# Optimization experiments

Measured on AMD Instinct MI355X. Metric: run time of the kernel, lower is better.

The kernel has to match this reference:

```python
import jax, jax.numpy as jnp
import numpy as np

B, T, C, H = 64, 256, 384, 6
HS = C // H  # 64
EPS = 1e-3  # keras LayerNormalization default epsilon


def layernorm(x, gamma, beta):
    mu = jnp.mean(x, axis=-1, keepdims=True)
    var = jnp.var(x, axis=-1, keepdims=True)
    return (x - mu) * jax.lax.rsqrt(var + EPS) * gamma + beta


def setup_inputs() -> dict:
    key = jax.random.key(0)
    ks = jax.random.split(key, 12)
    s = lambda fan_in: 1.0 / np.sqrt(fan_in)
    return {
        "x": jax.random.normal(ks[0], (B, T, C), dtype=jnp.float32),
        "Wq": jax.random.normal(ks[1], (H, C, HS), dtype=jnp.float32) * s(C),
        "Wk": jax.random.normal(ks[2], (H, C, HS), dtype=jnp.float32) * s(C),
        "Wv": jax.random.normal(ks[3], (H, C, HS), dtype=jnp.float32) * s(C),
        "Wp": jax.random.normal(ks[4], (C, C), dtype=jnp.float32) * s(C),
        "bp": jnp.zeros((C,), dtype=jnp.float32),
        "W1": jax.random.normal(ks[5], (C, 4 * C), dtype=jnp.float32) * s(C),
        "b1": jnp.zeros((4 * C,), dtype=jnp.float32),
        "W2": jax.random.normal(ks[6], (4 * C, C), dtype=jnp.float32) * s(4 * C),
        "b2": jnp.zeros((C,), dtype=jnp.float32),
        "g1": jnp.ones((C,), dtype=jnp.float32),
        "be1": jnp.zeros((C,), dtype=jnp.float32),
        "g2": jnp.ones((C,), dtype=jnp.float32),
        "be2": jnp.zeros((C,), dtype=jnp.float32),
    }


def reference(x, Wq, Wk, Wv, Wp, bp, W1, b1, W2, b2, g1, be1, g2, be2):
    # --- self-attention sub-block (dropout is identity at inference) ---
    h = layernorm(x, g1, be1)                              # [B,T,C]
    q = jnp.einsum('btc,hcd->bhtd', h, Wq)                 # [B,H,T,HS]
    k = jnp.einsum('btc,hcd->bhtd', h, Wk)
    v = jnp.einsum('btc,hcd->bhtd', h, Wv)
    scale = HS ** -0.5
    wei = jnp.einsum('bhtd,bhsd->bhts', q, k) * scale      # [B,H,T,T]
    causal = jnp.tril(jnp.ones((T, T), dtype=bool))
    wei = jnp.where(causal[None, None], wei, -jnp.inf)
    att = jax.nn.softmax(wei, axis=-1)
    o = jnp.einsum('bhts,bhsd->bthd', att, v).reshape(B, T, C)  # concat heads
    sa = o @ Wp + bp
    x = x + sa
    # --- feed-forward sub-block ---
    h2 = layernorm(x, g2, be2)
    ff = jax.nn.relu(h2 @ W1 + b1) @ W2 + b2
    return x + ff
```

## Files before the change

kernel.cpp:

```cpp
#include <hip/hip_runtime.h>
#include <hip/hip_bf16.h>
#include <math.h>

#define Bn 64
#define Tn 256
#define Cn 384
#define Hn 6
#define HSn 64
#define FFn 1536
#define EPSn 1e-3f
#define SECn 6291456

typedef __attribute__((ext_vector_type(4))) float f32x4;
typedef __attribute__((ext_vector_type(2))) float f32x2;
typedef __attribute__((ext_vector_type(8))) short short8;
typedef __attribute__((ext_vector_type(4))) short short4v;
typedef __attribute__((ext_vector_type(2))) short short2v;

__device__ __forceinline__ void async_copy16(void* lds, const void* g) {
    __builtin_amdgcn_global_load_lds(
        (const __attribute__((address_space(1))) void*)g,
        (__attribute__((address_space(3))) void*)lds, 16, 0, 0);
}

__device__ __forceinline__ short f2bf(float v) {
    __hip_bfloat16 h = __float2bfloat16(v);
    return *(short*)&h;
}


__global__ __launch_bounds__(256) void ln_pack_kernel(const float* __restrict__ x,
                                                      const float* __restrict__ g,
                                                      const float* __restrict__ be,
                                                      __hip_bfloat16* __restrict__ outPk) {
    int mt = blockIdx.x;
    int tid = threadIdx.x;
    int lane = tid & 63, wave = tid >> 6;
    __shared__ short rows[16 * 392];
#pragma unroll
    for (int i = 0; i < 4; i++) {
        int r = wave * 4 + i;
        const float* xr = x + ((size_t)mt * 16 + r) * Cn;
        f32x4 a = *(const f32x4*)(xr + lane * 4);
        f32x2 b = *(const f32x2*)(xr + 256 + lane * 2);
        float s = a.x + a.y + a.z + a.w + b.x + b.y;
#pragma unroll
        for (int off = 32; off; off >>= 1) s += __shfl_xor(s, off);
        float mu = s * (1.0f / Cn);
        f32x4 da = a - mu;
        f32x2 db = b - mu;
        float sq = da.x * da.x + da.y * da.y + da.z * da.z + da.w * da.w + db.x * db.x + db.y * db.y;
#pragma unroll
        for (int off = 32; off; off >>= 1) sq += __shfl_xor(sq, off);
        float rs = rsqrtf(sq * (1.0f / Cn) + EPSn);
        f32x4 g4 = *(const f32x4*)(g + lane * 4);
        f32x2 g2 = *(const f32x2*)(g + 256 + lane * 2);
        f32x4 e4 = *(const f32x4*)(be + lane * 4);
        f32x2 e2 = *(const f32x2*)(be + 256 + lane * 2);
        f32x4 y4 = da * rs * g4 + e4;
        f32x2 y2 = db * rs * g2 + e2;
        short4v o4 = {f2bf(y4.x), f2bf(y4.y), f2bf(y4.z), f2bf(y4.w)};
        *(short4v*)(&rows[r * 392 + lane * 4]) = o4;
        short2v o2 = {f2bf(y2.x), f2bf(y2.y)};
        *(short2v*)(&rows[r * 392 + 256 + lane * 2]) = o2;
    }
    __syncthreads();
    int r = lane & 15, q = lane >> 4;
#pragma unroll
    for (int p = 0; p < 3; p++) {
        int f = p * 4 + (tid >> 6);
        short8 v = *(const short8*)(&rows[r * 392 + f * 32 + q * 8]);
        *(short8*)((short*)outPk + ((size_t)mt * 12 + f) * 512 + lane * 8) = v;
    }
}

__global__ __launch_bounds__(256) void pack_b_kernel(const float* __restrict__ W,
                                                     __hip_bfloat16* __restrict__ out,
                                                     int K, int N) {
    int id = blockIdx.x * 256 + threadIdx.x;
    if (id >= K * N) return;
    int tile = id >> 9, lane = (id >> 3) & 63, j = id & 7;
    int ntiles = N >> 4;
    int k = (tile / ntiles) * 32 + ((lane >> 4) << 3) + j;
    int n = (tile % ntiles) * 16 + (lane & 15);
    out[id] = __float2bfloat16(W[(size_t)k * N + n]);
}

__global__ __launch_bounds__(256) void pack_qkv_kernel(const float* __restrict__ Wq,
                                                       const float* __restrict__ Wk,
                                                       const float* __restrict__ Wv,
                                                       __hip_bfloat16* __restrict__ out) {
    int id = blockIdx.x * 256 + threadIdx.x;
    if (id >= Cn * 1152) return;
    int tile = id >> 9, lane = (id >> 3) & 63, j = id & 7;
    int k = (tile / 72) * 32 + ((lane >> 4) << 3) + j;
    int n = (tile % 72) * 16 + (lane & 15);
    int sec = n / Cn, rem = n % Cn;
    int hh = rem >> 6, d = rem & 63;
    const float* W = (sec == 0) ? Wq : ((sec == 1) ? Wk : Wv);
    out[id] = __float2bfloat16(W[((size_t)hh * Cn + k) * HSn + d]);
}

template <int NN, int EPI>
__global__ __launch_bounds__(256, 3) void gemm_persist(const __hip_bfloat16* __restrict__ Apk,
                                                       const __hip_bfloat16* __restrict__ Bp,
                                                       const float* __restrict__ bias,
                                                       const float* __restrict__ resid,
                                                       float* __restrict__ outF,
                                                       __hip_bfloat16* __restrict__ outB) {
    constexpr int GX = NN / 64;
    constexpr int K32 = 12;
    constexpr int NT16 = NN / 16;
    __shared__ __align__(16) short ldsB[48 * 512];

    int l = blockIdx.x;
    int xcd = l & 7, i = l >> 3;
    int rowblk = xcd * 16 + i / GX;
    int colblk = i - (i / GX) * GX;

    int lane = threadIdx.x & 63, wave = threadIdx.x >> 6;
    int lrow = lane & 15, lquad = lane >> 4;
    int m0 = rowblk * 128;
    int n0 = colblk * 64;
    int mt0 = (m0 >> 4) + wave * 2;

    {
        const short* bbase = (const short*)Bp + (size_t)(n0 >> 4) * 512 + lane * 8;
#pragma unroll
        for (int t = 0; t < 12; t++) {
            int idx = wave * 12 + t;
            int kf = idx >> 2, ntl = idx & 3;
            async_copy16(&ldsB[idx * 512], bbase + ((size_t)kf * NT16 + ntl) * 512);
        }
    }

    f32x4 acc[2][4];
#pragma unroll
    for (int st = 0; st < 2; st++)
#pragma unroll
        for (int nt = 0; nt < 4; nt++) acc[st][nt] = (f32x4){0.f, 0.f, 0.f, 0.f};

    const short* a0p = (const short*)Apk + ((size_t)mt0 * K32) * 512 + lane * 8;
    const short* a1p = a0p + (size_t)K32 * 512;

    short8 af[2][2][3];
#pragma unroll
    for (int kf = 0; kf < 3; kf++) {
        af[0][0][kf] = *(const short8*)(a0p + kf * 512);
        af[0][1][kf] = *(const short8*)(a1p + kf * 512);
    }
    __syncthreads();

#pragma unroll
    for (int q = 0; q < 4; q++) {
        if (q < 3) {
#pragma unroll
            for (int kf = 0; kf < 3; kf++) {
                af[(q + 1) & 1][0][kf] = *(const short8*)(a0p + ((q + 1) * 3 + kf) * 512);
                af[(q + 1) & 1][1][kf] = *(const short8*)(a1p + ((q + 1) * 3 + kf) * 512);
            }
        }
#pragma unroll
        for (int kf = 0; kf < 3; kf++) {
            int kfa = q * 3 + kf;
#pragma unroll
            for (int nt = 0; nt < 4; nt++) {
                short8 bf = *(const short8*)(&ldsB[(kfa * 4 + nt) * 512 + lane * 8]);
                acc[0][nt] = __builtin_amdgcn_mfma_f32_16x16x32_bf16(af[q & 1][0][kf], bf,
                                                                     acc[0][nt], 0, 0, 0);
                acc[1][nt] = __builtin_amdgcn_mfma_f32_16x16x32_bf16(af[q & 1][1][kf], bf,
                                                                     acc[1][nt], 0, 0, 0);
            }
        }
    }
    __syncthreads();

    if (EPI == 1) {
        float* twf = (float*)((char*)ldsB + wave * 4864);
        float bnv[4];
#pragma unroll
        for (int nt = 0; nt < 4; nt++) bnv[nt] = bias[n0 + nt * 16 + lrow];
#pragma unroll
        for (int st = 0; st < 2; st++) {
            int mbase = m0 + (2 * wave + st) * 16;
#pragma unroll
            for (int nt = 0; nt < 4; nt++)
#pragma unroll
                for (int r = 0; r < 4; r++)
                    twf[(lquad * 4 + r) * 76 + nt * 16 + lrow] = acc[st][nt][r] + bnv[nt];
            int row = lane >> 2, seg = lane & 3;
            int m = mbase + row;
            const float* rrow = resid + (size_t)m * NN + n0 + seg * 16;
            float* orow = outF + (size_t)m * NN + n0 + seg * 16;
#pragma unroll
            for (int c = 0; c < 4; c++) {
                f32x4 vv = *(const f32x4*)(&twf[row * 76 + seg * 16 + c * 4]);
                f32x4 rv = *(const f32x4*)(rrow + c * 4);
                *(f32x4*)(orow + c * 4) = vv + rv;
            }
            __builtin_amdgcn_s_waitcnt(0);
        }
    } else {
        short* tws = (short*)((char*)ldsB + wave * 4864);
        float bnv[4];
        if (EPI == 2) {
#pragma unroll
            for (int nt = 0; nt < 4; nt++) bnv[nt] = bias[n0 + nt * 16 + lrow];
        }
#pragma unroll
        for (int st = 0; st < 2; st++)
#pragma unroll
            for (int nt = 0; nt < 4; nt++)
#pragma unroll
                for (int r = 0; r < 4; r++) {
                    float v = acc[st][nt][r];
                    if (EPI == 2) v = fmaxf(v + bnv[nt], 0.0f);
                    tws[(st * 16 + lquad * 4 + r) * 72 + nt * 16 + lrow] = f2bf(v);
                }
        if (EPI == 2) {
#pragma unroll
            for (int st2 = 0; st2 < 2; st2++) {
                int mt = (m0 >> 4) + wave * 2 + st2;
#pragma unroll
                for (int kcl = 0; kcl < 2; kcl++) {
                    int kc = (n0 >> 5) + kcl;
                    short8 v = *(const short8*)(
                        &tws[(st2 * 16 + (lane & 15)) * 72 + kcl * 32 + (lane >> 4) * 8]);
                    *(short8*)((short*)outB + ((size_t)mt * (NN / 32) + kc) * 512 + lane * 8) = v;
                }
            }
        } else {
            int sec = n0 / 384;
            int rem0 = n0 - sec * 384;
            int hh = rem0 >> 6;
            int b = m0 >> 8;
            int t_base = (m0 & 255) + wave * 32;
            int bh2 = b * Hn + hh;
            if (sec < 2) {
                short* outp = (short*)outB + (size_t)sec * SECn + (size_t)bh2 * 16384 +
                              (size_t)(t_base >> 4) * 1024 + lane * 8;
#pragma unroll
                for (int st2 = 0; st2 < 2; st2++)
#pragma unroll
                    for (int kc = 0; kc < 2; kc++) {
                        short8 v8 = *(const short8*)(
                            &tws[(st2 * 16 + (lane & 15)) * 72 + kc * 32 + (lane >> 4) * 8]);
                        *(short8*)(outp + (st2 * 2 + kc) * 512) = v8;
                    }
            } else {
                short* vout = (short*)outB + (size_t)2 * SECn + (size_t)bh2 * 16384 +
                              (size_t)((t_base >> 5) * 4) * 512;
#pragma unroll
                for (int dt = 0; dt < 4; dt++) {
                    short8 v8;
#pragma unroll
                    for (int j = 0; j < 8; j++) {
                        int t_loc = ((lane >> 4) << 3) + j;
                        v8[j] = tws[t_loc * 72 + dt * 16 + (lane & 15)];
                    }
                    *(short8*)(vout + dt * 512 + lane * 8) = v8;
                }
            }
        }
    }
}

template <int KK, int NN, int EPI>
__global__ __launch_bounds__(256) void gemm_mfma(const __hip_bfloat16* __restrict__ Apk,
                                                 const __hip_bfloat16* __restrict__ Bp,
                                                 const float* __restrict__ bias,
                                                 const float* __restrict__ resid,
                                                 float* __restrict__ outF,
                                                 __hip_bfloat16* __restrict__ outB) {
    constexpr int GX = NN / 64;
    constexpr int K32 = KK / 32;
    constexpr int NC = K32 / 4;
    constexpr int NT16 = NN / 16;
    __shared__ __align__(16) short ldsB[2 * 8192];

    int l = blockIdx.x;
    int xcd = l & 7, i = l >> 3;
    int rowblk = xcd * 16 + i / GX;
    int colblk = i - (i / GX) * GX;

    int lane = threadIdx.x & 63, wave = threadIdx.x >> 6;
    int lrow = lane & 15, lquad = lane >> 4;
    int m0 = rowblk * 128;
    int n0 = colblk * 64;
    int mt0 = (m0 >> 4) + wave * 2;

    f32x4 acc[2][4];
#pragma unroll
    for (int st = 0; st < 2; st++)
#pragma unroll
        for (int nt = 0; nt < 4; nt++) acc[st][nt] = (f32x4){0.f, 0.f, 0.f, 0.f};

    const short* a0p = (const short*)Apk + ((size_t)mt0 * K32) * 512 + lane * 8;
    const short* a1p = a0p + (size_t)K32 * 512;
    const short* bsrc = (const short*)Bp + ((size_t)wave * NT16 + (n0 >> 4)) * 512 + lane * 8;
    short* bdst0 = ldsB + wave * 2048;

#pragma unroll
    for (int nt = 0; nt < 4; nt++) async_copy16(bdst0 + nt * 512, bsrc + nt * 512);
    short8 aR[2][2][4];
#pragma unroll
    for (int kf = 0; kf < 4; kf++) {
        aR[0][0][kf] = *(const short8*)(a0p + kf * 512);
        aR[0][1][kf] = *(const short8*)(a1p + kf * 512);
    }

#pragma unroll
    for (int c = 0; c < NC; c++) {
        __syncthreads();
        if (c + 1 < NC) {
            const short* bs = bsrc + (size_t)(c + 1) * 4 * NT16 * 512;
            short* bd = ldsB + ((c + 1) & 1) * 8192 + wave * 2048;
#pragma unroll
            for (int nt = 0; nt < 4; nt++) async_copy16(bd + nt * 512, bs + nt * 512);
#pragma unroll
            for (int kf = 0; kf < 4; kf++) {
                aR[(c + 1) & 1][0][kf] = *(const short8*)(a0p + ((c + 1) * 4 + kf) * 512);
                aR[(c + 1) & 1][1][kf] = *(const short8*)(a1p + ((c + 1) * 4 + kf) * 512);
            }
        }
        const short* bl = ldsB + (c & 1) * 8192 + lane * 8;
#pragma unroll
        for (int kf = 0; kf < 4; kf++) {
#pragma unroll
            for (int nt = 0; nt < 4; nt++) {
                short8 bf = *(const short8*)(bl + (kf * 4 + nt) * 512);
                acc[0][nt] = __builtin_amdgcn_mfma_f32_16x16x32_bf16(aR[c & 1][0][kf], bf,
                                                                     acc[0][nt], 0, 0, 0);
                acc[1][nt] = __builtin_amdgcn_mfma_f32_16x16x32_bf16(aR[c & 1][1][kf], bf,
                                                                     acc[1][nt], 0, 0, 0);
            }
        }
    }
    __syncthreads();

    if (EPI == 1) {
        float* twf = (float*)((char*)ldsB + wave * 4864);
        float bnv[4];
#pragma unroll
        for (int nt = 0; nt < 4; nt++) bnv[nt] = bias[n0 + nt * 16 + lrow];
#pragma unroll
        for (int st = 0; st < 2; st++) {
            int mbase = m0 + (2 * wave + st) * 16;
#pragma unroll
            for (int nt = 0; nt < 4; nt++)
#pragma unroll
                for (int r = 0; r < 4; r++)
                    twf[(lquad * 4 + r) * 76 + nt * 16 + lrow] = acc[st][nt][r] + bnv[nt];
            int row = lane >> 2, seg = lane & 3;
            int m = mbase + row;
            const float* rrow = resid + (size_t)m * NN + n0 + seg * 16;
            float* orow = outF + (size_t)m * NN + n0 + seg * 16;
#pragma unroll
            for (int c = 0; c < 4; c++) {
                f32x4 vv = *(const f32x4*)(&twf[row * 76 + seg * 16 + c * 4]);
                f32x4 rv = *(const f32x4*)(rrow + c * 4);
                *(f32x4*)(orow + c * 4) = vv + rv;
            }
            __builtin_amdgcn_s_waitcnt(0);
        }
    } else {
        short* tws = (short*)((char*)ldsB + wave * 4864);
        float bnv[4];
        if (EPI == 2) {
#pragma unroll
            for (int nt = 0; nt < 4; nt++) bnv[nt] = bias[n0 + nt * 16 + lrow];
        }
#pragma unroll
        for (int st = 0; st < 2; st++)
#pragma unroll
            for (int nt = 0; nt < 4; nt++)
#pragma unroll
                for (int r = 0; r < 4; r++) {
                    float v = acc[st][nt][r];
                    if (EPI == 2) v = fmaxf(v + bnv[nt], 0.0f);
                    tws[(st * 16 + lquad * 4 + r) * 72 + nt * 16 + lrow] = f2bf(v);
                }
        if (EPI == 2) {
#pragma unroll
            for (int st2 = 0; st2 < 2; st2++) {
                int mt = (m0 >> 4) + wave * 2 + st2;
#pragma unroll
                for (int kcl = 0; kcl < 2; kcl++) {
                    int kc = (n0 >> 5) + kcl;
                    short8 v = *(const short8*)(
                        &tws[(st2 * 16 + (lane & 15)) * 72 + kcl * 32 + (lane >> 4) * 8]);
                    *(short8*)((short*)outB + ((size_t)mt * (NN / 32) + kc) * 512 + lane * 8) = v;
                }
            }
        }
    }
}

__global__ __launch_bounds__(256) void attn_mfma_kernel(const __hip_bfloat16* __restrict__ qp,
                                                        const __hip_bfloat16* __restrict__ kp,
                                                        const __hip_bfloat16* __restrict__ vp,
                                                        __hip_bfloat16* __restrict__ o) {
    __shared__ short Kl[16 * 1024];
    __shared__ short Pl[4 * 2048];
    int blk = blockIdx.x;
    int bh = blk % (Bn * Hn);
    int jg = blk / (Bn * Hn);
    int b = bh / Hn, hh = bh - b * Hn;
    int tid = threadIdx.x;
    int lane = tid & 63, wave = tid >> 6;
    int c16 = lane & 15, quad = lane >> 4;
    int qt = (wave << 2) + ((wave & 1) ? (3 - jg) : jg);

    const short* ks = (const short*)kp + (size_t)bh * 16384;
#pragma unroll
    for (int i = 0; i < 8; i++) {
        int tile = wave * 8 + i;
        async_copy16(&Kl[tile * 512], ks + tile * 512 + lane * 8);
    }

    const short* qs = (const short*)qp + (size_t)bh * 16384 + (size_t)qt * 1024 + lane * 8;
    const short* vs = (const short*)vp + (size_t)bh * 16384 + lane * 8;
    short* Pw = Pl + wave * 2048;

    short8 aq0 = *(const short8*)(qs);
    short8 aq1 = *(const short8*)(qs + 512);

    int st_max = qt;
    int kb_count = (qt + 2) >> 1;
    int covered = kb_count * 2;
    int qrow0 = qt * 16;

    __syncthreads();

    f32x4 accS[16];
#pragma unroll
    for (int st = 0; st < 16; st++) accS[st] = (f32x4){0.f, 0.f, 0.f, 0.f};
#pragma unroll
    for (int st = 0; st < 16; st++) {
        if (st <= st_max) {
            short8 bk0 = *(const short8*)(&Kl[st * 1024 + lane * 8]);
            short8 bk1 = *(const short8*)(&Kl[st * 1024 + 512 + lane * 8]);
            accS[st] = __builtin_amdgcn_mfma_f32_16x16x32_bf16(aq0, bk0, accS[st], 0, 0, 0);
            accS[st] = __builtin_amdgcn_mfma_f32_16x16x32_bf16(aq1, bk1, accS[st], 0, 0, 0);
        }
    }

    float mx[4];
#pragma unroll
    for (int r = 0; r < 4; r++) {
        int row = qrow0 + quad * 4 + r;
        float m = -INFINITY;
#pragma unroll
        for (int st = 0; st < 16; st++) {
            if (st <= st_max) {
                int col = st * 16 + c16;
                float a = (col <= row) ? accS[st][r] * 0.125f : -INFINITY;
                accS[st][r] = a;
                m = fmaxf(m, a);
            }
        }
#pragma unroll
        for (int off = 8; off; off >>= 1) m = fmaxf(m, __shfl_xor(m, off));
        mx[r] = m;
    }

    float sum[4] = {0.f, 0.f, 0.f, 0.f};
    f32x4 accO[4];
#pragma unroll
    for (int nt = 0; nt < 4; nt++) accO[nt] = (f32x4){0.f, 0.f, 0.f, 0.f};
#pragma unroll
    for (int half = 0; half < 2; half++) {
        int st_lo = half * 8;
        if (st_lo < covered) {
#pragma unroll
            for (int st2 = 0; st2 < 8; st2++) {
                int st = st_lo + st2;
                if (st < covered) {
#pragma unroll
                    for (int r = 0; r < 4; r++) {
                        float e = 0.0f;
                        if (st <= st_max) {
                            e = __expf(accS[st][r] - mx[r]);
                            sum[r] += e;
                        }
                        int cl = st2 * 16 + c16;
                        Pw[(cl >> 5) * 512 + (((cl >> 3) & 3) * 16 + quad * 4 + r) * 8 +
                           (cl & 7)] = f2bf(e);
                    }
                }
            }
#pragma unroll
            for (int k2 = 0; k2 < 4; k2++) {
                int kbi = half * 4 + k2;
                if (kbi < kb_count) {
                    short8 ap = *(const short8*)(Pw + k2 * 512 + lane * 8);
#pragma unroll
                    for (int nt = 0; nt < 4; nt++) {
                        short8 bv = *(const short8*)(vs + (kbi * 4 + nt) * 512);
                        accO[nt] = __builtin_amdgcn_mfma_f32_16x16x32_bf16(ap, bv, accO[nt],
                                                                           0, 0, 0);
                    }
                }
            }
        }
    }

    float inv[4];
#pragma unroll
    for (int r = 0; r < 4; r++) {
        float s = sum[r];
#pragma unroll
        for (int off = 8; off; off >>= 1) s += __shfl_xor(s, off);
        inv[r] = 1.0f / s;
    }

#pragma unroll
    for (int nt = 0; nt < 4; nt++)
#pragma unroll
        for (int r = 0; r < 4; r++)
            Pw[(quad * 4 + r) * 72 + nt * 16 + c16] = f2bf(accO[nt][r] * inv[r]);
    int mt = (b << 4) + qt;
#pragma unroll
    for (int kcl = 0; kcl < 2; kcl++) {
        short8 v = *(const short8*)(&Pw[(lane & 15) * 72 + kcl * 32 + (lane >> 4) * 8]);
        *(short8*)((short*)o + ((size_t)mt * 12 + hh * 2 + kcl) * 512 + lane * 8) = v;
    }
}

extern "C" void kernel_launch(void* const* d_in, const int* in_sizes, int n_in,
                              void* d_out, int out_size, void* d_ws, size_t ws_size,
                              hipStream_t stream) {
    const float* x  = (const float*)d_in[0];
    const float* Wq = (const float*)d_in[1];
    const float* Wk = (const float*)d_in[2];
    const float* Wv = (const float*)d_in[3];
    const float* Wp = (const float*)d_in[4];
    const float* bp = (const float*)d_in[5];
    const float* W1 = (const float*)d_in[6];
    const float* b1 = (const float*)d_in[7];
    const float* W2 = (const float*)d_in[8];
    const float* b2 = (const float*)d_in[9];
    const float* g1 = (const float*)d_in[10];
    const float* be1 = (const float*)d_in[11];
    const float* g2 = (const float*)d_in[12];
    const float* be2 = (const float*)d_in[13];

    const size_t M = (size_t)Bn * Tn;
    __hip_bfloat16* ws  = (__hip_bfloat16*)d_ws;
    __hip_bfloat16* h   = ws;
    __hip_bfloat16* big = h + M * Cn;
    __hip_bfloat16* o   = big + M * FFn;
    __hip_bfloat16* pQKV = o + M * Cn;
    __hip_bfloat16* pWp  = pQKV + Cn * 1152;
    __hip_bfloat16* pW1  = pWp + Cn * Cn;
    __hip_bfloat16* pW2  = pW1 + Cn * FFn;

    float* x2 = (float*)d_out;

    pack_qkv_kernel<<<(Cn * 1152 + 255) / 256, 256, 0, stream>>>(Wq, Wk, Wv, pQKV);
    pack_b_kernel<<<(Cn * Cn + 255) / 256, 256, 0, stream>>>(Wp, pWp, Cn, Cn);
    pack_b_kernel<<<(Cn * FFn + 255) / 256, 256, 0, stream>>>(W1, pW1, Cn, FFn);
    pack_b_kernel<<<(FFn * Cn + 255) / 256, 256, 0, stream>>>(W2, pW2, FFn, Cn);

    ln_pack_kernel<<<M / 16, 256, 0, stream>>>(x, g1, be1, h);
    gemm_persist<1152, 0><<<2304, 256, 0, stream>>>(h, pQKV, nullptr, nullptr, nullptr, big);
    attn_mfma_kernel<<<Bn * Hn * 4, 256, 0, stream>>>(big, big + SECn, big + 2 * SECn, o);
    gemm_persist<Cn, 1><<<768, 256, 0, stream>>>(o, pWp, bp, x, x2, nullptr);
    ln_pack_kernel<<<M / 16, 256, 0, stream>>>(x2, g2, be2, h);
    gemm_persist<FFn, 2><<<3072, 256, 0, stream>>>(h, pW1, b1, nullptr, nullptr, big);
    gemm_mfma<FFn, Cn, 1><<<768, 256, 0, stream>>>(big, pW2, b2, x2, x2, nullptr);
}
```

Baseline: 247.1 us.

## Merge weight packing into one launch and make attention query-tile grouping contiguous

The four weight-packing launches are merged into a single kernel that branches on a flat element index, removing three launch overheads. The attention kernel now gives each block four consecutive query tiles, with the heaviest group dispatched first, and loads only the causally needed K tiles instead of the full K sequence. The point is to skip K loads that causal masking never uses and to start long-running blocks early. In exchange, blocks are no longer balanced against each other, because each former block paired short and long query tiles to even out the work.

```diff
diff --git a/kernel.cpp b/kernel.cpp
--- a/kernel.cpp
+++ b/kernel.cpp
@@ -74,11 +74,8 @@
     }
 }
 
-__global__ __launch_bounds__(256) void pack_b_kernel(const float* __restrict__ W,
-                                                     __hip_bfloat16* __restrict__ out,
-                                                     int K, int N) {
-    int id = blockIdx.x * 256 + threadIdx.x;
-    if (id >= K * N) return;
+__device__ __forceinline__ void pack_b_one(const float* __restrict__ W,
+                                           __hip_bfloat16* __restrict__ out, int N, int id) {
     int tile = id >> 9, lane = (id >> 3) & 63, j = id & 7;
     int ntiles = N >> 4;
     int k = (tile / ntiles) * 32 + ((lane >> 4) << 3) + j;
@@ -86,19 +83,32 @@
     out[id] = __float2bfloat16(W[(size_t)k * N + n]);
 }
 
-__global__ __launch_bounds__(256) void pack_qkv_kernel(const float* __restrict__ Wq,
-                                                       const float* __restrict__ Wk,
-                                                       const float* __restrict__ Wv,
-                                                       __hip_bfloat16* __restrict__ out) {
+#define QKV_E 442368
+#define WP_E  147456
+#define W1_E  589824
+#define W2_E  589824
+
+__global__ __launch_bounds__(256) void pack_all_kernel(
+    const float* __restrict__ Wq, const float* __restrict__ Wk, const float* __restrict__ Wv,
+    const float* __restrict__ Wp, const float* __restrict__ W1, const float* __restrict__ W2,
+    __hip_bfloat16* __restrict__ pQKV, __hip_bfloat16* __restrict__ pWp,
+    __hip_bfloat16* __restrict__ pW1, __hip_bfloat16* __restrict__ pW2) {
     int id = blockIdx.x * 256 + threadIdx.x;
-    if (id >= Cn * 1152) return;
-    int tile = id >> 9, lane = (id >> 3) & 63, j = id & 7;
-    int k = (tile / 72) * 32 + ((lane >> 4) << 3) + j;
-    int n = (tile % 72) * 16 + (lane & 15);
-    int sec = n / Cn, rem = n % Cn;
-    int hh = rem >> 6, d = rem & 63;
-    const float* W = (sec == 0) ? Wq : ((sec == 1) ? Wk : Wv);
-    out[id] = __float2bfloat16(W[((size_t)hh * Cn + k) * HSn + d]);
+    if (id < QKV_E) {
+        int tile = id >> 9, lane = (id >> 3) & 63, j = id & 7;
+        int k = (tile / 72) * 32 + ((lane >> 4) << 3) + j;
+        int n = (tile % 72) * 16 + (lane & 15);
+        int sec = n / Cn, rem = n % Cn;
+        int hh = rem >> 6, d = rem & 63;
+        const float* W = (sec == 0) ? Wq : ((sec == 1) ? Wk : Wv);
+        pQKV[id] = __float2bfloat16(W[((size_t)hh * Cn + k) * HSn + d]);
+    } else if (id < QKV_E + WP_E) {
+        pack_b_one(Wp, pWp, Cn, id - QKV_E);
+    } else if (id < QKV_E + WP_E + W1_E) {
+        pack_b_one(W1, pW1, FFn, id - (QKV_E + WP_E));
+    } else {
+        pack_b_one(W2, pW2, Cn, id - (QKV_E + WP_E + W1_E));
+    }
 }
 
 template <int NN, int EPI>
@@ -404,18 +414,22 @@
     __shared__ short Pl[4 * 2048];
     int blk = blockIdx.x;
     int bh = blk % (Bn * Hn);
-    int jg = blk / (Bn * Hn);
+    int jgr = 3 - blk / (Bn * Hn);
     int b = bh / Hn, hh = bh - b * Hn;
     int tid = threadIdx.x;
     int lane = tid & 63, wave = tid >> 6;
     int c16 = lane & 15, quad = lane >> 4;
-    int qt = (wave << 2) + ((wave & 1) ? (3 - jg) : jg);
+    int qt = (jgr << 2) + wave;
 
     const short* ks = (const short*)kp + (size_t)bh * 16384;
-#pragma unroll
-    for (int i = 0; i < 8; i++) {
-        int tile = wave * 8 + i;
-        async_copy16(&Kl[tile * 512], ks + tile * 512 + lane * 8);
+    int per = jgr + 1;
+#pragma unroll
+    for (int i = 0; i < 4; i++) {
+        if (i < per) {
+            int tile = wave * per + i;
+            async_copy16(&Kl[tile * 1024], ks + tile * 1024 + lane * 8);
+            async_copy16(&Kl[tile * 1024 + 512], ks + tile * 1024 + 512 + lane * 8);
+        }
     }
 
     const short* qs = (const short*)qp + (size_t)bh * 16384 + (size_t)qt * 1024 + lane * 8;
@@ -557,10 +571,8 @@
 
     float* x2 = (float*)d_out;
 
-    pack_qkv_kernel<<<(Cn * 1152 + 255) / 256, 256, 0, stream>>>(Wq, Wk, Wv, pQKV);
-    pack_b_kernel<<<(Cn * Cn + 255) / 256, 256, 0, stream>>>(Wp, pWp, Cn, Cn);
-    pack_b_kernel<<<(Cn * FFn + 255) / 256, 256, 0, stream>>>(W1, pW1, Cn, FFn);
-    pack_b_kernel<<<(FFn * Cn + 255) / 256, 256, 0, stream>>>(W2, pW2, FFn, Cn);
+    pack_all_kernel<<<(QKV_E + WP_E + W1_E + W2_E) / 256, 256, 0, stream>>>(
+        Wq, Wk, Wv, Wp, W1, W2, pQKV, pWp, pW1, pW2);
 
     ln_pack_kernel<<<M / 16, 256, 0, stream>>>(x, g1, be1, h);
     gemm_persist<1152, 0><<<2304, 256, 0, stream>>>(h, pQKV, nullptr, nullptr, nullptr, big);
```

Measured after the change: 235.1 us. -4.9%, faster.
